# Optimization experiments

Measured on AMD Instinct MI355X. Metric: run time of the kernel, lower is better.

## Reference

```python
import jax, jax.numpy as jnp
import numpy as np

N = 50000      # nodes
E = 800000     # edges (avg degree 16)
IN = 128       # in_channels = len(cfg.objects)
OC = 16        # out_channels
DIMS = [IN, 16 * OC, 8 * OC, 4 * OC, 2 * OC, OC]  # 128,256,128,64,32,16


def _glorot(key, fan_in, fan_out):
    s = jnp.sqrt(2.0 / (fan_in + fan_out)).astype(jnp.float32)
    return jax.random.normal(key, (fan_in, fan_out), jnp.float32) * s


def setup_inputs() -> dict:
    key = jax.random.key(0)
    ks = jax.random.split(key, 16)
    x = jax.random.normal(ks[0], (N, IN), jnp.float32)
    edge_index = jax.random.randint(ks[1], (2, E), 0, N, dtype=jnp.int32)
    inp = {"x": x, "edge_index": edge_index}
    # four hidden GCN layers
    names = ["1", "2", "3", "4"]
    for i, nm in enumerate(names):
        inp["W" + nm] = _glorot(ks[2 + i], DIMS[i], DIMS[i + 1])
        inp["b" + nm] = jnp.zeros((DIMS[i + 1],), jnp.float32)
    # mu / logstd heads
    inp["Wmu"] = _glorot(ks[10], DIMS[4], DIMS[5])
    inp["bmu"] = jnp.zeros((DIMS[5],), jnp.float32)
    inp["Wls"] = _glorot(ks[11], DIMS[4], DIMS[5])
    inp["bls"] = jnp.zeros((DIMS[5],), jnp.float32)
    return inp


def _gcn_norm(edge_index, n):
    # GCNConv default: add self-loops, symmetric normalization
    sl = jnp.arange(n, dtype=edge_index.dtype)
    row = jnp.concatenate([edge_index[0], sl])  # source
    col = jnp.concatenate([edge_index[1], sl])  # target
    deg = jax.ops.segment_sum(jnp.ones_like(row, jnp.float32), col, num_segments=n)
    dinv = jnp.where(deg > 0, jax.lax.rsqrt(deg), 0.0)
    norm = dinv[row] * dinv[col]  # [E + N]
    return row, col, norm


def _gcn_conv(x, W, b, row, col, norm, n):
    h = x @ W                                   # dense transform [N, F_out]
    msg = h[row] * norm[:, None]                # gather + edge scale
    return jax.ops.segment_sum(msg, col, num_segments=n) + b  # scatter-add


def reference(x, edge_index, W1, b1, W2, b2, W3, b3, W4, b4, Wmu, bmu, Wls, bls):
    n = x.shape[0]
    row, col, norm = _gcn_norm(edge_index, n)
    h = jax.nn.relu(_gcn_conv(x, W1, b1, row, col, norm, n))
    h = jax.nn.relu(_gcn_conv(h, W2, b2, row, col, norm, n))
    h = jax.nn.relu(_gcn_conv(h, W3, b3, row, col, norm, n))
    h = jax.nn.relu(_gcn_conv(h, W4, b4, row, col, norm, n))
    mu = _gcn_conv(h, Wmu, bmu, row, col, norm, n)
    logstd = _gcn_conv(h, Wls, bls, row, col, norm, n)
    return mu, logstd
```

## Files before the change

### kernel.cpp

```cpp
#include <hip/hip_runtime.h>
#include <hip/hip_bf16.h>
#include <stdint.h>

__device__ inline int imin(int a, int b) { return a < b ? a : b; }
__device__ inline int imax(int a, int b) { return a > b ? a : b; }
__device__ inline float bf2f(unsigned short u) {
    return __uint_as_float(((unsigned int)u) << 16);
}
__device__ inline unsigned short f2bf(float v) {
    unsigned int u = __float_as_uint(v);
    unsigned int r = u + 0x7FFFu + ((u >> 16) & 1u);
    return (unsigned short)(r >> 16);
}

typedef __attribute__((ext_vector_type(8))) short short8;
typedef __attribute__((ext_vector_type(4))) float floatx4;


__global__ void k_zero_i32(int* __restrict__ p, int n) {
    int i = blockIdx.x * blockDim.x + threadIdx.x;
    if (i < n) p[i] = 0;
}

__global__ void k_count(const int* __restrict__ col, int* __restrict__ cnt, int E, int n) {
    int e = blockIdx.x * blockDim.x + threadIdx.x;
    if (e < E) {
        int c = imax(0, imin(col[e], n - 1));
        atomicAdd(&cnt[c], 1);
    }
}

__global__ __launch_bounds__(256) void k_scan1(const int* __restrict__ cnt,
                                               int* __restrict__ partial,
                                               int* __restrict__ bsum, int n) {
    __shared__ int tmp[256];
    int i = blockIdx.x * 256 + threadIdx.x;
    int v = (i < n) ? ((cnt[i] + 3) & ~3) : 0;
    tmp[threadIdx.x] = v;
    __syncthreads();
    #pragma unroll
    for (int s = 1; s < 256; s <<= 1) {
        int t = (threadIdx.x >= s) ? tmp[threadIdx.x - s] : 0;
        __syncthreads();
        tmp[threadIdx.x] += t;
        __syncthreads();
    }
    if (i < n) partial[i] = tmp[threadIdx.x] - v;
    if (threadIdx.x == 255) bsum[blockIdx.x] = tmp[255];
}

__global__ __launch_bounds__(256) void k_scan2(const int* __restrict__ bsum,
                                               int* __restrict__ bsumoff, int nb) {
    __shared__ int tmp[256];
    __shared__ int carry;
    if (threadIdx.x == 0) carry = 0;
    __syncthreads();
    for (int base = 0; base < nb; base += 256) {
        int i = base + threadIdx.x;
        int v = (i < nb) ? bsum[i] : 0;
        tmp[threadIdx.x] = v;
        __syncthreads();
        #pragma unroll
        for (int s = 1; s < 256; s <<= 1) {
            int t = (threadIdx.x >= s) ? tmp[threadIdx.x - s] : 0;
            __syncthreads();
            tmp[threadIdx.x] += t;
            __syncthreads();
        }
        if (i < nb) bsumoff[i] = carry + tmp[threadIdx.x] - v;
        __syncthreads();
        if (threadIdx.x == 0) carry += tmp[255];
        __syncthreads();
    }
}

__global__ __launch_bounds__(256) void k_scan3(const int* __restrict__ partial,
                                               const int* __restrict__ bsumoff,
                                               const int* __restrict__ cnt,
                                               int* __restrict__ offs, int* __restrict__ cursor,
                                               float* __restrict__ dinv, int n) {
    int i = blockIdx.x * 256 + threadIdx.x;
    if (i >= n) return;
    int v = partial[i] + bsumoff[blockIdx.x];
    offs[i] = v;
    cursor[i] = v;
    if (i == n - 1) offs[n] = v + ((cnt[i] + 3) & ~3);
    float d = (float)imax(cnt[i], 0) + 1.0f;
    dinv[i] = rsqrtf(d);
}

template <bool USEW>
__global__ void k_fill(const int* __restrict__ row, const int* __restrict__ col,
                       int* __restrict__ cursor, const float* __restrict__ dinv,
                       uint2* __restrict__ edges, int* __restrict__ csr_src,
                       int E, int n, int cap) {
    int e = blockIdx.x * blockDim.x + threadIdx.x;
    if (e >= E) return;
    int c = imax(0, imin(col[e], n - 1));
    int r = imax(0, imin(row[e], n - 1));
    int pos = atomicAdd(&cursor[c], 1);
    pos = imax(0, imin(pos, cap - 1));
    if (USEW) {
        uint2 rec;
        rec.x = (unsigned)r;
        rec.y = __float_as_uint(dinv[r]);
        edges[pos] = rec;
    } else {
        csr_src[pos] = r;
    }
}

template <bool USEW>
__global__ void k_pad(const int* __restrict__ cnt, const int* __restrict__ offs,
                      const int* __restrict__ cursor,
                      uint2* __restrict__ edges, int* __restrict__ csr_src, int n) {
    int i = blockIdx.x * blockDim.x + threadIdx.x;
    if (i >= n) return;
    int end = offs[i] + ((cnt[i] + 3) & ~3);
    for (int p = cursor[i]; p < end; p++) {
        if (USEW) edges[p] = make_uint2(0u, 0u);
        else csr_src[p] = 0;
    }
}


__global__ void k_cvt_bf(const float* __restrict__ in, unsigned short* __restrict__ out, size_t n) {
    size_t i = (size_t)blockIdx.x * 256 + threadIdx.x;
    if (i < n) out[i] = f2bf(in[i]);
}

__global__ void k_wcast3(const float* __restrict__ W1, unsigned short* __restrict__ W1T,
                         const float* __restrict__ W2, unsigned short* __restrict__ W2T,
                         const float* __restrict__ W3, unsigned short* __restrict__ W3T) {
    int idx = blockIdx.x * 256 + threadIdx.x;
    const int n1 = 128 * 256, n2 = 256 * 128, n3 = 128 * 64;
    if (idx < n1) {
        int k = idx >> 8, n = idx & 255;
        W1T[n * 128 + k] = f2bf(W1[idx]);
    } else if (idx < n1 + n2) {
        int j = idx - n1;
        int k = j >> 7, n = j & 127;
        W2T[n * 256 + k] = f2bf(W2[j]);
    } else if (idx < n1 + n2 + n3) {
        int j = idx - n1 - n2;
        int k = j >> 6, n = j & 63;
        W3T[n * 128 + k] = f2bf(W3[j]);
    }
}


template <int NT, int FOUT, bool EPI>
__global__ __launch_bounds__(256) void k_gemm_mfma(const unsigned short* __restrict__ act,
                                                   const unsigned short* __restrict__ WT,
                                                   unsigned short* __restrict__ H,
                                                   const float* __restrict__ bias,
                                                   int nrows, int Fin) {
    constexpr int CT = NT / 16;
    __shared__ __align__(16) unsigned short sA[128 * 40];
    __shared__ __align__(16) unsigned short sB[NT * 40];
    const int tid = threadIdx.x;
    const int w = tid >> 6;
    const int lane = tid & 63;
    const int quad = lane >> 4;
    const int l15 = lane & 15;
    const int row0 = blockIdx.x * 128;
    const int col0 = blockIdx.y * NT;

    floatx4 acc[2][CT] = {};

    const int sr = tid >> 1;
    const int sp = (tid & 1) * 16;

    for (int k0 = 0; k0 < Fin; k0 += 32) {
        __syncthreads();
        {
            int grow = row0 + sr;
            uint4 v0 = make_uint4(0, 0, 0, 0), v1 = make_uint4(0, 0, 0, 0);
            if (grow < nrows) {
                const uint4* ap = (const uint4*)&act[(size_t)grow * Fin + k0 + sp];
                v0 = ap[0]; v1 = ap[1];
            }
            uint4* dst = (uint4*)&sA[sr * 40 + sp];
            dst[0] = v0; dst[1] = v1;
        }
        if (NT == 128 || tid < 128) {
            const uint4* wp = (const uint4*)&WT[(size_t)(col0 + sr) * Fin + k0 + sp];
            uint4* dst = (uint4*)&sB[sr * 40 + sp];
            dst[0] = wp[0]; dst[1] = wp[1];
        }
        __syncthreads();

        short8 bfr[CT];
        #pragma unroll
        for (int ct = 0; ct < CT; ct++)
            bfr[ct] = *(const short8*)&sB[(ct * 16 + l15) * 40 + quad * 8];
        #pragma unroll
        for (int rt = 0; rt < 2; rt++) {
            short8 afr = *(const short8*)&sA[(w * 32 + rt * 16 + l15) * 40 + quad * 8];
            #pragma unroll
            for (int ct = 0; ct < CT; ct++)
                acc[rt][ct] = __builtin_amdgcn_mfma_f32_16x16x32_bf16(afr, bfr[ct], acc[rt][ct], 0, 0, 0);
        }
    }

    #pragma unroll
    for (int rt = 0; rt < 2; rt++) {
        #pragma unroll
        for (int ct = 0; ct < CT; ct++) {
            int gcol = col0 + ct * 16 + l15;
            #pragma unroll
            for (int r = 0; r < 4; r++) {
                int grow = row0 + w * 32 + rt * 16 + quad * 4 + r;
                if (grow < nrows) {
                    float v = acc[rt][ct][r];
                    if (EPI) v = fmaxf(v + bias[gcol], 0.f);
                    H[(size_t)grow * FOUT + gcol] = f2bf(v);
                }
            }
        }
    }
}


__global__ __launch_bounds__(256) void k_gemm32(const unsigned short* __restrict__ act,
                                                const float* __restrict__ W,
                                                unsigned short* __restrict__ H,
                                                int nrows) {
    __shared__ __align__(16) float sA[32 * 68];
    __shared__ __align__(16) float sW[16 * 32];
    const int tid = threadIdx.x;
    const int row0 = blockIdx.x * 32;
    const int Fin = 64, strA = 68;

    for (int i = tid; i < 32 * Fin; i += 256) {
        int r = i >> 6;
        int k = i & 63;
        float v = 0.f;
        if (row0 + r < nrows) v = bf2f(act[(size_t)row0 * Fin + i]);
        sA[r * strA + k] = v;
    }

    const int rl = tid >> 3;
    const int cg = tid & 7;
    float a0 = 0.f, a1 = 0.f, a2 = 0.f, a3 = 0.f;

    for (int k0 = 0; k0 < Fin; k0 += 16) {
        __syncthreads();
        const float* wsrc = W + (size_t)k0 * 32;
        for (int i = tid; i < 16 * 32; i += 256) sW[i] = wsrc[i];
        __syncthreads();
        #pragma unroll 4
        for (int kk = 0; kk < 16; kk++) {
            float a = sA[rl * strA + k0 + kk];
            float4 wv = *(const float4*)&sW[kk * 32 + cg * 4];
            a0 = fmaf(a, wv.x, a0);
            a1 = fmaf(a, wv.y, a1);
            a2 = fmaf(a, wv.z, a2);
            a3 = fmaf(a, wv.w, a3);
        }
    }

    const int rowi = row0 + rl;
    if (rowi < nrows) {
        unsigned short* hp = &H[(size_t)rowi * 32 + cg * 4];
        hp[0] = f2bf(a0); hp[1] = f2bf(a1); hp[2] = f2bf(a2); hp[3] = f2bf(a3);
    }
}

__global__ void k_gemm_heads(const unsigned short* __restrict__ act,
                             const float* __restrict__ Wmu, const float* __restrict__ Wls,
                             unsigned short* __restrict__ H, int nrows) {
    int idx = blockIdx.x * blockDim.x + threadIdx.x;
    if (idx >= nrows * 32) return;
    int r = idx >> 5;
    int c = idx & 31;
    const float* Wp = (c < 16) ? Wmu : Wls;
    int cc = c & 15;
    float acc = 0.f;
    #pragma unroll 8
    for (int k = 0; k < 32; k++)
        acc = fmaf(bf2f(act[(size_t)r * 32 + k]), Wp[k * 16 + cc], acc);
    H[idx] = f2bf(acc);
}


template <int F, bool RELU, bool HASBIAS, bool USEW>
__global__ __launch_bounds__(256) void k_aggb(const unsigned short* __restrict__ Hb,
                                              unsigned short* __restrict__ out,
                                              const int* __restrict__ offs,
                                              const uint2* __restrict__ edges,
                                              const int* __restrict__ src,
                                              const float* __restrict__ dinv,
                                              const float* __restrict__ bias,
                                              int nnodes, int Ecap) {
    constexpr int TPN = (F >= 128) ? 64 : F / 2;
    int t = blockIdx.x * 256 + threadIdx.x;
    int node = t / TPN;
    int ln = t % TPN;
    if (node >= nnodes) return;
    int f0 = 2 * ln;

    float di = dinv[node];
    ushort2 sv = *(const ushort2*)&Hb[(size_t)node * F + f0];
    float acc0 = di * bf2f(sv.x);
    float acc1 = di * bf2f(sv.y);

    int s0 = offs[node];
    int s1 = offs[node + 1];
    s0 = imax(0, imin(s0, Ecap));
    s1 = imax(s0, imin(s1, Ecap));
    for (int e = s0; e < s1; e += 4) {
        int sr0, sr1, sr2, sr3;
        float w0, w1, w2, w3;
        if (USEW) {
            uint4 p0 = *(const uint4*)(edges + e);
            uint4 p1 = *(const uint4*)(edges + e + 2);
            sr0 = (int)p0.x; w0 = __uint_as_float(p0.y);
            sr1 = (int)p0.z; w1 = __uint_as_float(p0.w);
            sr2 = (int)p1.x; w2 = __uint_as_float(p1.y);
            sr3 = (int)p1.z; w3 = __uint_as_float(p1.w);
        } else {
            const int4 sr4 = *(const int4*)(src + e);
            sr0 = sr4.x; sr1 = sr4.y; sr2 = sr4.z; sr3 = sr4.w;
            w0 = dinv[sr0]; w1 = dinv[sr1]; w2 = dinv[sr2]; w3 = dinv[sr3];
        }
        ushort2 h0 = *(const ushort2*)&Hb[(size_t)sr0 * F + f0];
        ushort2 h1 = *(const ushort2*)&Hb[(size_t)sr1 * F + f0];
        ushort2 h2 = *(const ushort2*)&Hb[(size_t)sr2 * F + f0];
        ushort2 h3 = *(const ushort2*)&Hb[(size_t)sr3 * F + f0];
        acc0 = fmaf(w0, bf2f(h0.x), acc0);
        acc1 = fmaf(w0, bf2f(h0.y), acc1);
        acc0 = fmaf(w1, bf2f(h1.x), acc0);
        acc1 = fmaf(w1, bf2f(h1.y), acc1);
        acc0 = fmaf(w2, bf2f(h2.x), acc0);
        acc1 = fmaf(w2, bf2f(h2.y), acc1);
        acc0 = fmaf(w3, bf2f(h3.x), acc0);
        acc1 = fmaf(w3, bf2f(h3.y), acc1);
    }
    float v0 = di * acc0;
    float v1 = di * acc1;
    if (HASBIAS) { v0 += bias[f0]; v1 += bias[f0 + 1]; }
    if (RELU) { v0 = fmaxf(v0, 0.f); v1 = fmaxf(v1, 0.f); }
    ushort2 o; o.x = f2bf(v0); o.y = f2bf(v1);
    *(ushort2*)&out[(size_t)node * F + f0] = o;
}

template <bool USEW>
__global__ __launch_bounds__(256) void k_agg_heads(const unsigned short* __restrict__ Hb,
                                                   float* __restrict__ out,
                                                   const int* __restrict__ offs,
                                                   const uint2* __restrict__ edges,
                                                   const int* __restrict__ src,
                                                   const float* __restrict__ dinv,
                                                   const float* __restrict__ bmu, const float* __restrict__ bls,
                                                   int nnodes, int Ecap) {
    constexpr int F = 32, TPN = 16;
    int t = blockIdx.x * 256 + threadIdx.x;
    int node = t / TPN;
    int ln = t % TPN;
    if (node >= nnodes) return;
    int f0 = 2 * ln;

    float di = dinv[node];
    ushort2 sv = *(const ushort2*)&Hb[(size_t)node * F + f0];
    float acc0 = di * bf2f(sv.x);
    float acc1 = di * bf2f(sv.y);

    int s0 = offs[node];
    int s1 = offs[node + 1];
    s0 = imax(0, imin(s0, Ecap));
    s1 = imax(s0, imin(s1, Ecap));
    for (int e = s0; e < s1; e += 4) {
        int sr0, sr1, sr2, sr3;
        float w0, w1, w2, w3;
        if (USEW) {
            uint4 p0 = *(const uint4*)(edges + e);
            uint4 p1 = *(const uint4*)(edges + e + 2);
            sr0 = (int)p0.x; w0 = __uint_as_float(p0.y);
            sr1 = (int)p0.z; w1 = __uint_as_float(p0.w);
            sr2 = (int)p1.x; w2 = __uint_as_float(p1.y);
            sr3 = (int)p1.z; w3 = __uint_as_float(p1.w);
        } else {
            const int4 sr4 = *(const int4*)(src + e);
            sr0 = sr4.x; sr1 = sr4.y; sr2 = sr4.z; sr3 = sr4.w;
            w0 = dinv[sr0]; w1 = dinv[sr1]; w2 = dinv[sr2]; w3 = dinv[sr3];
        }
        ushort2 h0 = *(const ushort2*)&Hb[(size_t)sr0 * F + f0];
        ushort2 h1 = *(const ushort2*)&Hb[(size_t)sr1 * F + f0];
        ushort2 h2 = *(const ushort2*)&Hb[(size_t)sr2 * F + f0];
        ushort2 h3 = *(const ushort2*)&Hb[(size_t)sr3 * F + f0];
        acc0 = fmaf(w0, bf2f(h0.x), acc0);
        acc1 = fmaf(w0, bf2f(h0.y), acc1);
        acc0 = fmaf(w1, bf2f(h1.x), acc0);
        acc1 = fmaf(w1, bf2f(h1.y), acc1);
        acc0 = fmaf(w2, bf2f(h2.x), acc0);
        acc1 = fmaf(w2, bf2f(h2.y), acc1);
        acc0 = fmaf(w3, bf2f(h3.x), acc0);
        acc1 = fmaf(w3, bf2f(h3.y), acc1);
    }
    const float* bp = (f0 < 16) ? bmu : bls;
    int fb = f0 & 15;
    float v0 = fmaf(di, acc0, bp[fb]);
    float v1 = fmaf(di, acc1, bp[fb + 1]);
    float* op = (f0 < 16) ? (out + (size_t)node * 16 + fb)
                          : (out + (size_t)nnodes * 16 + (size_t)node * 16 + fb);
    *(float2*)op = make_float2(v0, v1);
}


template <bool USEW>
static void run_pipeline(void* const* d_in, void* d_out, void* d_ws,
                         int N, int E, hipStream_t stream) {
    const float* x  = (const float*)d_in[0];
    const int* ei   = (const int*)d_in[1];
    const float* W1 = (const float*)d_in[2];
    const float* b1 = (const float*)d_in[3];
    const float* W2 = (const float*)d_in[4];
    const float* b2 = (const float*)d_in[5];
    const float* W3 = (const float*)d_in[6];
    const float* b3 = (const float*)d_in[7];
    const float* W4 = (const float*)d_in[8];
    const float* b4 = (const float*)d_in[9];
    const float* Wmu = (const float*)d_in[10];
    const float* bmu = (const float*)d_in[11];
    const float* Wls = (const float*)d_in[12];
    const float* bls = (const float*)d_in[13];
    const int* row = ei;
    const int* col = ei + E;
    const int nb = (N + 255) / 256;
    const int E4 = E + 4 * N;

    auto align16 = [](char* p) {
        return (char*)(((uintptr_t)p + 15) & ~(uintptr_t)15);
    };
    char* p = (char*)d_ws;
    unsigned short* act = (unsigned short*)p;    p += (size_t)N * 256 * 2;
    unsigned short* H = (unsigned short*)p;      p += (size_t)N * 256 * 2;
    unsigned short* xb = H;
    unsigned short* xa = (unsigned short*)p;     p += (size_t)N * 128 * 2;
    float* dinv = (float*)p;                     p += (size_t)N * 4;
    int* cnt = (int*)p;                          p += (size_t)N * 4;
    int* offs = (int*)p;                         p += (size_t)(N + 1) * 4;
    int* cursor = (int*)p;                       p += (size_t)N * 4;
    int* partial = (int*)p;                      p += (size_t)N * 4;
    int* bsum = (int*)p;                         p += (size_t)nb * 4;
    int* bsumoff = (int*)p;                      p += (size_t)nb * 4;
    p = align16(p);
    unsigned short* W1T = (unsigned short*)p;    p += 256 * 128 * 2;
    unsigned short* W2T = (unsigned short*)p;    p += 128 * 256 * 2;
    unsigned short* W3T = (unsigned short*)p;    p += 64 * 128 * 2;
    p = align16(p);
    uint2* edges = nullptr;
    int* csr_src = nullptr;
    if (USEW) edges = (uint2*)p;
    else      csr_src = (int*)p;

    k_zero_i32<<<nb, 256, 0, stream>>>(cnt, N);
    k_count<<<(E + 255) / 256, 256, 0, stream>>>(col, cnt, E, N);
    k_scan1<<<nb, 256, 0, stream>>>(cnt, partial, bsum, N);
    k_scan2<<<1, 256, 0, stream>>>(bsum, bsumoff, nb);
    k_scan3<<<nb, 256, 0, stream>>>(partial, bsumoff, cnt, offs, cursor, dinv, N);
    k_fill<USEW><<<(E + 255) / 256, 256, 0, stream>>>(row, col, cursor, dinv, edges, csr_src, E, N, E4);
    k_pad<USEW><<<nb, 256, 0, stream>>>(cnt, offs, cursor, edges, csr_src, N);

    k_wcast3<<<(128 * 256 + 256 * 128 + 128 * 64 + 255) / 256, 256, 0, stream>>>(W1, W1T, W2, W2T, W3, W3T);

    const int gx = (N + 127) / 128;
    k_cvt_bf<<<(unsigned)(((size_t)N * 128 + 255) / 256), 256, 0, stream>>>(x, xb, (size_t)N * 128);
    k_aggb<128, false, false, USEW><<<(unsigned)(((size_t)N * 64 + 255) / 256), 256, 0, stream>>>(xb, xa, offs, edges, csr_src, dinv, nullptr, N, E4);
    k_gemm_mfma<128, 256, true><<<dim3(gx, 2), 256, 0, stream>>>(xa, W1T, act, b1, N, 128);
    k_gemm_mfma<128, 128, false><<<dim3(gx, 1), 256, 0, stream>>>(act, W2T, H, nullptr, N, 256);
    k_aggb<128, true, true, USEW><<<(unsigned)(((size_t)N * 64 + 255) / 256), 256, 0, stream>>>(H, act, offs, edges, csr_src, dinv, b2, N, E4);
    k_gemm_mfma<64, 64, false><<<dim3(gx, 1), 256, 0, stream>>>(act, W3T, H, nullptr, N, 128);
    k_aggb<64, true, true, USEW><<<(unsigned)(((size_t)N * 32 + 255) / 256), 256, 0, stream>>>(H, act, offs, edges, csr_src, dinv, b3, N, E4);
    k_gemm32<<<(N + 31) / 32, 256, 0, stream>>>(act, W4, H, N);
    k_aggb<32, true, true, USEW><<<(unsigned)(((size_t)N * 16 + 255) / 256), 256, 0, stream>>>(H, act, offs, edges, csr_src, dinv, b4, N, E4);
    float* outF = (float*)d_out;
    k_gemm_heads<<<(unsigned)(((size_t)N * 32 + 255) / 256), 256, 0, stream>>>(act, Wmu, Wls, H, N);
    k_agg_heads<USEW><<<(unsigned)(((size_t)N * 16 + 255) / 256), 256, 0, stream>>>(H, outF, offs, edges, csr_src, dinv, bmu, bls, N, E4);
}

extern "C" void kernel_launch(void* const* d_in, const int* in_sizes, int n_in,
                              void* d_out, int out_size, void* d_ws, size_t ws_size,
                              hipStream_t stream) {
    const int N = in_sizes[0] / 128;
    const int E = in_sizes[1] / 2;
    const int nb = (N + 255) / 256;
    const size_t E4 = (size_t)E + 4 * (size_t)N;

    size_t fixed = (size_t)N * 256 * 2 * 2 + (size_t)N * 128 * 2
                 + (size_t)N * 4 * 5 + 4 + (size_t)nb * 8
                 + (256 * 128 + 128 * 256 + 64 * 128) * 2 + 96;
    size_t need_w = fixed + E4 * 8;
    if (ws_size >= need_w)
        run_pipeline<true>(d_in, d_out, d_ws, N, E, stream);
    else
        run_pipeline<false>(d_in, d_out, d_ws, N, E, stream);
}
```

Before: 393.3 us.

## Fuse prologue kernels, pad CSR rows to eight, unroll aggregation by eight

Merges count zeroing, input bf16 conversion and weight transposes into a single prologue launch. k_count and k_fill now handle two edges per thread. CSR rows are padded to multiples of 8 instead of 4, and the gather-aggregate loops are unrolled to 8 edges, putting more independent loads in flight per thread. The cost is more padding edges (up to 7 per node) to store and process, plus higher register pressure in the aggregation kernels.

```diff
diff --git a/kernel.cpp b/kernel.cpp
--- a/kernel.cpp
+++ b/kernel.cpp
@@ -17,15 +17,43 @@
 typedef __attribute__((ext_vector_type(4))) float floatx4;
 
 
-__global__ void k_zero_i32(int* __restrict__ p, int n) {
-    int i = blockIdx.x * blockDim.x + threadIdx.x;
-    if (i < n) p[i] = 0;
-}
+__global__ void k_prologue(int* __restrict__ cnt, int n,
+                           const float* __restrict__ x, unsigned short* __restrict__ xb, size_t nx,
+                           const float* __restrict__ W1, unsigned short* __restrict__ W1T,
+                           const float* __restrict__ W2, unsigned short* __restrict__ W2T,
+                           const float* __restrict__ W3, unsigned short* __restrict__ W3T) {
+    size_t i = (size_t)blockIdx.x * 256 + threadIdx.x;
+    if (i < (size_t)n) { cnt[i] = 0; }
+    size_t j = i - n;
+    if (i >= (size_t)n && j < nx) { xb[j] = f2bf(x[j]); }
+    size_t k = j - nx;
+    const int n1 = 128 * 256, n2 = 256 * 128, n3 = 128 * 64;
+    if (j >= nx && k < (size_t)(n1 + n2 + n3)) {
+        int idx = (int)k;
+        if (idx < n1) {
+            int kk = idx >> 8, nn = idx & 255;
+            W1T[nn * 128 + kk] = f2bf(W1[idx]);
+        } else if (idx < n1 + n2) {
+            int jj = idx - n1;
+            int kk = jj >> 7, nn = jj & 127;
+            W2T[nn * 256 + kk] = f2bf(W2[jj]);
+        } else {
+            int jj = idx - n1 - n2;
+            int kk = jj >> 6, nn = jj & 63;
+            W3T[nn * 128 + kk] = f2bf(W3[jj]);
+        }
+    }
+}
+
 
 __global__ void k_count(const int* __restrict__ col, int* __restrict__ cnt, int E, int n) {
-    int e = blockIdx.x * blockDim.x + threadIdx.x;
-    if (e < E) {
-        int c = imax(0, imin(col[e], n - 1));
+    int e0 = (blockIdx.x * blockDim.x + threadIdx.x) * 2;
+    if (e0 < E) {
+        int c = imax(0, imin(col[e0], n - 1));
+        atomicAdd(&cnt[c], 1);
+    }
+    if (e0 + 1 < E) {
+        int c = imax(0, imin(col[e0 + 1], n - 1));
         atomicAdd(&cnt[c], 1);
     }
 }
@@ -35,7 +63,7 @@
                                                int* __restrict__ bsum, int n) {
     __shared__ int tmp[256];
     int i = blockIdx.x * 256 + threadIdx.x;
-    int v = (i < n) ? ((cnt[i] + 3) & ~3) : 0;
+    int v = (i < n) ? ((cnt[i] + 7) & ~7) : 0;
     tmp[threadIdx.x] = v;
     __syncthreads();
     #pragma unroll
@@ -84,7 +112,7 @@
     int v = partial[i] + bsumoff[blockIdx.x];
     offs[i] = v;
     cursor[i] = v;
-    if (i == n - 1) offs[n] = v + ((cnt[i] + 3) & ~3);
+    if (i == n - 1) offs[n] = v + ((cnt[i] + 7) & ~7);
     float d = (float)imax(cnt[i], 0) + 1.0f;
     dinv[i] = rsqrtf(d);
 }
@@ -94,19 +122,23 @@
                        int* __restrict__ cursor, const float* __restrict__ dinv,
                        uint2* __restrict__ edges, int* __restrict__ csr_src,
                        int E, int n, int cap) {
-    int e = blockIdx.x * blockDim.x + threadIdx.x;
-    if (e >= E) return;
-    int c = imax(0, imin(col[e], n - 1));
-    int r = imax(0, imin(row[e], n - 1));
-    int pos = atomicAdd(&cursor[c], 1);
-    pos = imax(0, imin(pos, cap - 1));
-    if (USEW) {
-        uint2 rec;
-        rec.x = (unsigned)r;
-        rec.y = __float_as_uint(dinv[r]);
-        edges[pos] = rec;
-    } else {
-        csr_src[pos] = r;
+    int e0 = (blockIdx.x * blockDim.x + threadIdx.x) * 2;
+    #pragma unroll
+    for (int u = 0; u < 2; u++) {
+        int e = e0 + u;
+        if (e >= E) break;
+        int c = imax(0, imin(col[e], n - 1));
+        int r = imax(0, imin(row[e], n - 1));
+        int pos = atomicAdd(&cursor[c], 1);
+        pos = imax(0, imin(pos, cap - 1));
+        if (USEW) {
+            uint2 rec;
+            rec.x = (unsigned)r;
+            rec.y = __float_as_uint(dinv[r]);
+            edges[pos] = rec;
+        } else {
+            csr_src[pos] = r;
+        }
     }
 }
 
@@ -116,35 +148,10 @@
                       uint2* __restrict__ edges, int* __restrict__ csr_src, int n) {
     int i = blockIdx.x * blockDim.x + threadIdx.x;
     if (i >= n) return;
-    int end = offs[i] + ((cnt[i] + 3) & ~3);
+    int end = offs[i] + ((cnt[i] + 7) & ~7);
     for (int p = cursor[i]; p < end; p++) {
         if (USEW) edges[p] = make_uint2(0u, 0u);
         else csr_src[p] = 0;
-    }
-}
-
-
-__global__ void k_cvt_bf(const float* __restrict__ in, unsigned short* __restrict__ out, size_t n) {
-    size_t i = (size_t)blockIdx.x * 256 + threadIdx.x;
-    if (i < n) out[i] = f2bf(in[i]);
-}
-
-__global__ void k_wcast3(const float* __restrict__ W1, unsigned short* __restrict__ W1T,
-                         const float* __restrict__ W2, unsigned short* __restrict__ W2T,
-                         const float* __restrict__ W3, unsigned short* __restrict__ W3T) {
-    int idx = blockIdx.x * 256 + threadIdx.x;
-    const int n1 = 128 * 256, n2 = 256 * 128, n3 = 128 * 64;
-    if (idx < n1) {
-        int k = idx >> 8, n = idx & 255;
-        W1T[n * 128 + k] = f2bf(W1[idx]);
-    } else if (idx < n1 + n2) {
-        int j = idx - n1;
-        int k = j >> 7, n = j & 127;
-        W2T[n * 256 + k] = f2bf(W2[j]);
-    } else if (idx < n1 + n2 + n3) {
-        int j = idx - n1 - n2;
-        int k = j >> 6, n = j & 63;
-        W3T[n * 128 + k] = f2bf(W3[j]);
     }
 }
 
@@ -309,33 +316,33 @@
     int s1 = offs[node + 1];
     s0 = imax(0, imin(s0, Ecap));
     s1 = imax(s0, imin(s1, Ecap));
-    for (int e = s0; e < s1; e += 4) {
-        int sr0, sr1, sr2, sr3;
-        float w0, w1, w2, w3;
+    for (int e = s0; e < s1; e += 8) {
+        int sr[8];
+        float wv[8];
         if (USEW) {
-            uint4 p0 = *(const uint4*)(edges + e);
-            uint4 p1 = *(const uint4*)(edges + e + 2);
-            sr0 = (int)p0.x; w0 = __uint_as_float(p0.y);
-            sr1 = (int)p0.z; w1 = __uint_as_float(p0.w);
-            sr2 = (int)p1.x; w2 = __uint_as_float(p1.y);
-            sr3 = (int)p1.z; w3 = __uint_as_float(p1.w);
+            #pragma unroll
+            for (int q = 0; q < 4; q++) {
+                uint4 pr = *(const uint4*)(edges + e + 2 * q);
+                sr[2 * q] = (int)pr.x;     wv[2 * q] = __uint_as_float(pr.y);
+                sr[2 * q + 1] = (int)pr.z; wv[2 * q + 1] = __uint_as_float(pr.w);
+            }
         } else {
-            const int4 sr4 = *(const int4*)(src + e);
-            sr0 = sr4.x; sr1 = sr4.y; sr2 = sr4.z; sr3 = sr4.w;
-            w0 = dinv[sr0]; w1 = dinv[sr1]; w2 = dinv[sr2]; w3 = dinv[sr3];
-        }
-        ushort2 h0 = *(const ushort2*)&Hb[(size_t)sr0 * F + f0];
-        ushort2 h1 = *(const ushort2*)&Hb[(size_t)sr1 * F + f0];
-        ushort2 h2 = *(const ushort2*)&Hb[(size_t)sr2 * F + f0];
-        ushort2 h3 = *(const ushort2*)&Hb[(size_t)sr3 * F + f0];
-        acc0 = fmaf(w0, bf2f(h0.x), acc0);
-        acc1 = fmaf(w0, bf2f(h0.y), acc1);
-        acc0 = fmaf(w1, bf2f(h1.x), acc0);
-        acc1 = fmaf(w1, bf2f(h1.y), acc1);
-        acc0 = fmaf(w2, bf2f(h2.x), acc0);
-        acc1 = fmaf(w2, bf2f(h2.y), acc1);
-        acc0 = fmaf(w3, bf2f(h3.x), acc0);
-        acc1 = fmaf(w3, bf2f(h3.y), acc1);
+            int4 a = *(const int4*)(src + e);
+            int4 b = *(const int4*)(src + e + 4);
+            sr[0] = a.x; sr[1] = a.y; sr[2] = a.z; sr[3] = a.w;
+            sr[4] = b.x; sr[5] = b.y; sr[6] = b.z; sr[7] = b.w;
+            #pragma unroll
+            for (int q = 0; q < 8; q++) wv[q] = dinv[sr[q]];
+        }
+        ushort2 h[8];
+        #pragma unroll
+        for (int q = 0; q < 8; q++)
+            h[q] = *(const ushort2*)&Hb[(size_t)sr[q] * F + f0];
+        #pragma unroll
+        for (int q = 0; q < 8; q++) {
+            acc0 = fmaf(wv[q], bf2f(h[q].x), acc0);
+            acc1 = fmaf(wv[q], bf2f(h[q].y), acc1);
+        }
     }
     float v0 = di * acc0;
     float v1 = di * acc1;
@@ -370,33 +377,33 @@
     int s1 = offs[node + 1];
     s0 = imax(0, imin(s0, Ecap));
     s1 = imax(s0, imin(s1, Ecap));
-    for (int e = s0; e < s1; e += 4) {
-        int sr0, sr1, sr2, sr3;
-        float w0, w1, w2, w3;
+    for (int e = s0; e < s1; e += 8) {
+        int sr[8];
+        float wv[8];
         if (USEW) {
-            uint4 p0 = *(const uint4*)(edges + e);
-            uint4 p1 = *(const uint4*)(edges + e + 2);
-            sr0 = (int)p0.x; w0 = __uint_as_float(p0.y);
-            sr1 = (int)p0.z; w1 = __uint_as_float(p0.w);
-            sr2 = (int)p1.x; w2 = __uint_as_float(p1.y);
-            sr3 = (int)p1.z; w3 = __uint_as_float(p1.w);
+            #pragma unroll
+            for (int q = 0; q < 4; q++) {
+                uint4 pr = *(const uint4*)(edges + e + 2 * q);
+                sr[2 * q] = (int)pr.x;     wv[2 * q] = __uint_as_float(pr.y);
+                sr[2 * q + 1] = (int)pr.z; wv[2 * q + 1] = __uint_as_float(pr.w);
+            }
         } else {
-            const int4 sr4 = *(const int4*)(src + e);
-            sr0 = sr4.x; sr1 = sr4.y; sr2 = sr4.z; sr3 = sr4.w;
-            w0 = dinv[sr0]; w1 = dinv[sr1]; w2 = dinv[sr2]; w3 = dinv[sr3];
-        }
-        ushort2 h0 = *(const ushort2*)&Hb[(size_t)sr0 * F + f0];
-        ushort2 h1 = *(const ushort2*)&Hb[(size_t)sr1 * F + f0];
-        ushort2 h2 = *(const ushort2*)&Hb[(size_t)sr2 * F + f0];
-        ushort2 h3 = *(const ushort2*)&Hb[(size_t)sr3 * F + f0];
-        acc0 = fmaf(w0, bf2f(h0.x), acc0);
-        acc1 = fmaf(w0, bf2f(h0.y), acc1);
-        acc0 = fmaf(w1, bf2f(h1.x), acc0);
-        acc1 = fmaf(w1, bf2f(h1.y), acc1);
-        acc0 = fmaf(w2, bf2f(h2.x), acc0);
-        acc1 = fmaf(w2, bf2f(h2.y), acc1);
-        acc0 = fmaf(w3, bf2f(h3.x), acc0);
-        acc1 = fmaf(w3, bf2f(h3.y), acc1);
+            int4 a = *(const int4*)(src + e);
+            int4 b = *(const int4*)(src + e + 4);
+            sr[0] = a.x; sr[1] = a.y; sr[2] = a.z; sr[3] = a.w;
+            sr[4] = b.x; sr[5] = b.y; sr[6] = b.z; sr[7] = b.w;
+            #pragma unroll
+            for (int q = 0; q < 8; q++) wv[q] = dinv[sr[q]];
+        }
+        ushort2 h[8];
+        #pragma unroll
+        for (int q = 0; q < 8; q++)
+            h[q] = *(const ushort2*)&Hb[(size_t)sr[q] * F + f0];
+        #pragma unroll
+        for (int q = 0; q < 8; q++) {
+            acc0 = fmaf(wv[q], bf2f(h[q].x), acc0);
+            acc1 = fmaf(wv[q], bf2f(h[q].y), acc1);
+        }
     }
     const float* bp = (f0 < 16) ? bmu : bls;
     int fb = f0 & 15;
@@ -428,7 +435,7 @@
     const int* row = ei;
     const int* col = ei + E;
     const int nb = (N + 255) / 256;
-    const int E4 = E + 4 * N;
+    const int E8 = E + 8 * N;
 
     auto align16 = [](char* p) {
         return (char*)(((uintptr_t)p + 15) & ~(uintptr_t)15);
@@ -455,29 +462,30 @@
     if (USEW) edges = (uint2*)p;
     else      csr_src = (int*)p;
 
-    k_zero_i32<<<nb, 256, 0, stream>>>(cnt, N);
-    k_count<<<(E + 255) / 256, 256, 0, stream>>>(col, cnt, E, N);
+    {
+        size_t total = (size_t)N + (size_t)N * 128 + (128 * 256 + 256 * 128 + 128 * 64);
+        k_prologue<<<(unsigned)((total + 255) / 256), 256, 0, stream>>>(
+            cnt, N, x, xb, (size_t)N * 128, W1, W1T, W2, W2T, W3, W3T);
+    }
+    k_count<<<(E / 2 + 255) / 256, 256, 0, stream>>>(col, cnt, E, N);
     k_scan1<<<nb, 256, 0, stream>>>(cnt, partial, bsum, N);
     k_scan2<<<1, 256, 0, stream>>>(bsum, bsumoff, nb);
     k_scan3<<<nb, 256, 0, stream>>>(partial, bsumoff, cnt, offs, cursor, dinv, N);
-    k_fill<USEW><<<(E + 255) / 256, 256, 0, stream>>>(row, col, cursor, dinv, edges, csr_src, E, N, E4);
+    k_fill<USEW><<<(E / 2 + 255) / 256, 256, 0, stream>>>(row, col, cursor, dinv, edges, csr_src, E, N, E8);
     k_pad<USEW><<<nb, 256, 0, stream>>>(cnt, offs, cursor, edges, csr_src, N);
 
-    k_wcast3<<<(128 * 256 + 256 * 128 + 128 * 64 + 255) / 256, 256, 0, stream>>>(W1, W1T, W2, W2T, W3, W3T);
-
     const int gx = (N + 127) / 128;
-    k_cvt_bf<<<(unsigned)(((size_t)N * 128 + 255) / 256), 256, 0, stream>>>(x, xb, (size_t)N * 128);
-    k_aggb<128, false, false, USEW><<<(unsigned)(((size_t)N * 64 + 255) / 256), 256, 0, stream>>>(xb, xa, offs, edges, csr_src, dinv, nullptr, N, E4);
+    k_aggb<128, false, false, USEW><<<(unsigned)(((size_t)N * 64 + 255) / 256), 256, 0, stream>>>(xb, xa, offs, edges, csr_src, dinv, nullptr, N, E8);
     k_gemm_mfma<128, 256, true><<<dim3(gx, 2), 256, 0, stream>>>(xa, W1T, act, b1, N, 128);
     k_gemm_mfma<128, 128, false><<<dim3(gx, 1), 256, 0, stream>>>(act, W2T, H, nullptr, N, 256);
-    k_aggb<128, true, true, USEW><<<(unsigned)(((size_t)N * 64 + 255) / 256), 256, 0, stream>>>(H, act, offs, edges, csr_src, dinv, b2, N, E4);
+    k_aggb<128, true, true, USEW><<<(unsigned)(((size_t)N * 64 + 255) / 256), 256, 0, stream>>>(H, act, offs, edges, csr_src, dinv, b2, N, E8);
     k_gemm_mfma<64, 64, false><<<dim3(gx, 1), 256, 0, stream>>>(act, W3T, H, nullptr, N, 128);
-    k_aggb<64, true, true, USEW><<<(unsigned)(((size_t)N * 32 + 255) / 256), 256, 0, stream>>>(H, act, offs, edges, csr_src, dinv, b3, N, E4);
+    k_aggb<64, true, true, USEW><<<(unsigned)(((size_t)N * 32 + 255) / 256), 256, 0, stream>>>(H, act, offs, edges, csr_src, dinv, b3, N, E8);
     k_gemm32<<<(N + 31) / 32, 256, 0, stream>>>(act, W4, H, N);
-    k_aggb<32, true, true, USEW><<<(unsigned)(((size_t)N * 16 + 255) / 256), 256, 0, stream>>>(H, act, offs, edges, csr_src, dinv, b4, N, E4);
+    k_aggb<32, true, true, USEW><<<(unsigned)(((size_t)N * 16 + 255) / 256), 256, 0, stream>>>(H, act, offs, edges, csr_src, dinv, b4, N, E8);
     float* outF = (float*)d_out;
     k_gemm_heads<<<(unsigned)(((size_t)N * 32 + 255) / 256), 256, 0, stream>>>(act, Wmu, Wls, H, N);
-    k_agg_heads<USEW><<<(unsigned)(((size_t)N * 16 + 255) / 256), 256, 0, stream>>>(H, outF, offs, edges, csr_src, dinv, bmu, bls, N, E4);
+    k_agg_heads<USEW><<<(unsigned)(((size_t)N * 16 + 255) / 256), 256, 0, stream>>>(H, outF, offs, edges, csr_src, dinv, bmu, bls, N, E8);
 }
 
 extern "C" void kernel_launch(void* const* d_in, const int* in_sizes, int n_in,
@@ -486,12 +494,12 @@
     const int N = in_sizes[0] / 128;
     const int E = in_sizes[1] / 2;
     const int nb = (N + 255) / 256;
-    const size_t E4 = (size_t)E + 4 * (size_t)N;
+    const size_t E8 = (size_t)E + 8 * (size_t)N;
 
     size_t fixed = (size_t)N * 256 * 2 * 2 + (size_t)N * 128 * 2
                  + (size_t)N * 4 * 5 + 4 + (size_t)nb * 8
                  + (256 * 128 + 128 * 256 + 64 * 128) * 2 + 96;
-    size_t need_w = fixed + E4 * 8;
+    size_t need_w = fixed + E8 * 8;
     if (ws_size >= need_w)
         run_pipeline<true>(d_in, d_out, d_ws, N, E, stream);
     else
```

Measured after the change: 382.1 us. 1.03x faster.
